# Performance work log

Hardware: AMD Instinct MI355X
Metric: run time of the kernel (lower is better)

The kernel has to match this reference:

```python
import jax, jax.numpy as jnp
import numpy as np

N_NODES = 50000
N_EDGES = 800000
N_GRAPHS = 128
IN, HID, OUT, CLS = 128, 128, 128, 10


def setup_inputs() -> dict:
    key = jax.random.key(0)
    ks = jax.random.split(key, 16)
    d = {}
    d["features"] = jax.random.normal(ks[0], (N_NODES, IN), jnp.float32)
    d["edge_src"] = jax.random.randint(ks[1], (N_EDGES,), 0, N_NODES)
    d["edge_dst"] = jax.random.randint(ks[2], (N_EDGES,), 0, N_NODES)
    d["graph_ids"] = jnp.sort(jax.random.randint(ks[3], (N_NODES,), 0, N_GRAPHS))

    def lin(k, i, o):
        return (jax.random.normal(k, (i, o), jnp.float32) / np.float32(np.sqrt(i)))

    dims = [(IN, HID), (HID, HID), (HID, OUT)]
    for l, (i, o) in enumerate(dims):
        d[f"Ws{l}"] = lin(ks[4 + 3 * l], i, o)
        d[f"Wn{l}"] = lin(ks[5 + 3 * l], i, o)
        d[f"b{l}"] = jnp.zeros((o,), jnp.float32)
    d["Wf"] = lin(ks[13], OUT, CLS)
    d["bf"] = jnp.zeros((CLS,), jnp.float32)
    return d


def _sage_mean_layer(h, edge_src, edge_dst, Ws, Wn, b, in_deg):
    # mean-aggregate in-neighbor features: gather at src, segment-sum at dst
    msg_sum = jax.ops.segment_sum(h[edge_src], edge_dst, num_segments=N_NODES)
    h_neigh = msg_sum / in_deg  # [N, d], zero-degree nodes divide by 1 -> 0
    return jax.nn.relu(h @ Ws + h_neigh @ Wn + b)


def reference(features, edge_src, edge_dst, graph_ids,
              Ws0, Wn0, b0, Ws1, Wn1, b1, Ws2, Wn2, b2, Wf, bf):
    ones = jnp.ones((N_EDGES,), jnp.float32)
    in_deg = jax.ops.segment_sum(ones, edge_dst, num_segments=N_NODES)
    in_deg = jnp.maximum(in_deg, 1.0)[:, None]  # [N, 1]

    h = features
    h = _sage_mean_layer(h, edge_src, edge_dst, Ws0, Wn0, b0, in_deg)
    h = _sage_mean_layer(h, edge_src, edge_dst, Ws1, Wn1, b1, in_deg)
    h = _sage_mean_layer(h, edge_src, edge_dst, Ws2, Wn2, b2, in_deg)

    # mean graph pooling over node segments
    node_ones = jnp.ones((N_NODES,), jnp.float32)
    counts = jax.ops.segment_sum(node_ones, graph_ids, num_segments=N_GRAPHS)
    counts = jnp.maximum(counts, 1.0)[:, None]
    pooled = jax.ops.segment_sum(h, graph_ids, num_segments=N_GRAPHS) / counts

    return pooled @ Wf + bf  # [N_GRAPHS, CLS]
```

## Files before the change

### kernel.cpp

```cpp
#include <hip/hip_runtime.h>

#define N_NODES  50000
#define N_EDGES  800000
#define N_GRAPHS 128
#define HD       128
#define K2       256
#define CLS      10
#define NB_SCAN  ((N_NODES + 255) / 256)
#define NPART    8
#define PSIZE    (N_NODES / NPART)
#define NBIN     400
#define CHUNK    (N_EDGES / NBIN)
#define PCAP     131072

typedef __attribute__((ext_vector_type(8))) _Float16 f16x8;
typedef __attribute__((ext_vector_type(4))) float f32x4;
typedef __attribute__((ext_vector_type(2))) float f32x2;

union U4H8 { uint4 u; _Float16 h[8]; };
union U2H4 { uint2 u; _Float16 h[4]; };

__device__ inline float h2f(unsigned short s) {
    union { unsigned short u; _Float16 h; } c; c.u = s; return (float)c.h;
}

__global__ __launch_bounds__(256) void k_init(const float* __restrict__ f,
                                              unsigned short* __restrict__ c0, unsigned char* __restrict__ f8,
                                              const float* __restrict__ Ws0, const float* __restrict__ Wn0,
                                              const float* __restrict__ Ws1, const float* __restrict__ Wn1,
                                              const float* __restrict__ Ws2, const float* __restrict__ Wn2,
                                              unsigned short* __restrict__ wt,
                                              int* __restrict__ zero_region, float* __restrict__ pooled,
                                              const int* __restrict__ gid, float* __restrict__ counts) {
    long long gi = (long long)blockIdx.x * 256 + threadIdx.x;
    if (gi < 800000) {
        int t = (int)gi;
        int row = t >> 4, c8 = (t & 15) * 8;
        const float* p = f + (size_t)row * HD + c8;
        float4 a = *(const float4*)p;
        float4 b = *(const float4*)(p + 4);
        U4H8 v;
        v.h[0] = (_Float16)a.x; v.h[1] = (_Float16)a.y;
        v.h[2] = (_Float16)a.z; v.h[3] = (_Float16)a.w;
        v.h[4] = (_Float16)b.x; v.h[5] = (_Float16)b.y;
        v.h[6] = (_Float16)b.z; v.h[7] = (_Float16)b.w;
        *(uint4*)(c0 + (size_t)row * K2 + c8) = v.u;
        int p0 = __builtin_amdgcn_cvt_pk_fp8_f32(a.x, a.y, 0, false);
        p0 = __builtin_amdgcn_cvt_pk_fp8_f32(a.z, a.w, p0, true);
        int p1 = __builtin_amdgcn_cvt_pk_fp8_f32(b.x, b.y, 0, false);
        p1 = __builtin_amdgcn_cvt_pk_fp8_f32(b.z, b.w, p1, true);
        *(uint2*)(f8 + (size_t)row * HD + c8) = make_uint2((unsigned)p0, (unsigned)p1);
        return;
    }
    gi -= 800000;
    if (gi < 3 * HD * K2) {
        int t = (int)gi;
        int l = t / (HD * K2), r = t % (HD * K2);
        int n = r / K2, k = r % K2;
        const float* Ws = (l == 0) ? Ws0 : (l == 1) ? Ws1 : Ws2;
        const float* Wn = (l == 0) ? Wn0 : (l == 1) ? Wn1 : Wn2;
        float w = (k < HD) ? Ws[k * HD + n] : Wn[(k - HD) * HD + n];
        union { unsigned short u; _Float16 h; } c;
        c.h = (_Float16)w;
        wt[t] = c.u;
        return;
    }
    gi -= 3 * HD * K2;
    if (gi < 50064) { zero_region[gi] = 0; return; }
    gi -= 50064;
    if (gi < N_GRAPHS * HD) { pooled[gi] = 0.f; return; }
    gi -= (long long)N_GRAPHS * HD;
    if (gi < N_GRAPHS) {
        int g = (int)gi;
        int lo = 0, hi = N_NODES;
        while (lo < hi) { int mid = (lo + hi) >> 1; if (gid[mid] < g) lo = mid + 1; else hi = mid; }
        int start = lo;
        lo = 0; hi = N_NODES;
        while (lo < hi) { int mid = (lo + hi) >> 1; if (gid[mid] <= g) lo = mid + 1; else hi = mid; }
        counts[g] = (float)(lo - start);
    }
}
#define INIT_THREADS (800000 + 3 * HD * K2 + 50064 + N_GRAPHS * HD + N_GRAPHS)

__global__ __launch_bounds__(256) void k_bin(const int* __restrict__ src, const int* __restrict__ dst,
                                             int2* __restrict__ stag, int* __restrict__ gcount) {
    __shared__ int lcount[NPART];
    __shared__ int lbase[NPART];
    const int tid = threadIdx.x;
    const int lane = tid & 63;
    const int lo = blockIdx.x * CHUNK;
    if (tid < NPART) lcount[tid] = 0;
    __syncthreads();
    for (int i = lo + tid; i < lo + CHUNK; i += 256) {
        int p = dst[i] / PSIZE;
#pragma unroll
        for (int q = 0; q < NPART; ++q) {
            unsigned long long m = __ballot(p == q);
            if (p == q) {
                int leader = __ffsll((long long)m) - 1;
                if (lane == leader) atomicAdd(&lcount[q], (int)__popcll(m));
            }
        }
    }
    __syncthreads();
    if (tid < NPART) {
        lbase[tid] = atomicAdd(&gcount[tid], lcount[tid]);
        lcount[tid] = 0;
    }
    __syncthreads();
    for (int i = lo + tid; i < lo + CHUNK; i += 256) {
        int d = dst[i];
        int p = d / PSIZE;
        int slot = 0;
#pragma unroll
        for (int q = 0; q < NPART; ++q) {
            unsigned long long m = __ballot(p == q);
            if (p == q) {
                int leader = __ffsll((long long)m) - 1;
                int rank = (int)__popcll(m & ((1ull << lane) - 1ull));
                int base;
                if (lane == leader) base = atomicAdd(&lcount[q], (int)__popcll(m));
                base = __shfl(base, leader);
                slot = base + rank;
            }
        }
        stag[(size_t)p * PCAP + lbase[p] + slot] = make_int2(src[i], d);
    }
}

__global__ __launch_bounds__(256) void k_deg2(const int2* __restrict__ stag, const int* __restrict__ gcount,
                                              int* __restrict__ deg) {
    const int part = blockIdx.x & (NPART - 1);
    const int blk = blockIdx.x >> 3;
    const int n = gcount[part];
    const int2* s = stag + (size_t)part * PCAP;
    for (int i = blk * 256 + threadIdx.x; i < n; i += 64 * 256)
        atomicAdd(&deg[s[i].y], 1);
}

__global__ __launch_bounds__(256) void k_fill2(const int2* __restrict__ stag, const int* __restrict__ gcount,
                                               int* __restrict__ cursor, int* __restrict__ eidx) {
    const int part = blockIdx.x & (NPART - 1);
    const int blk = blockIdx.x >> 3;
    const int n = gcount[part];
    const int2* s = stag + (size_t)part * PCAP;
    for (int i = blk * 256 + threadIdx.x; i < n; i += 64 * 256) {
        int2 e = s[i];
        int pos = atomicAdd(&cursor[e.y], 1);
        eidx[pos] = e.x;
    }
}

__global__ __launch_bounds__(256) void k_scan_part(const int* __restrict__ deg,
                                                   int* __restrict__ rowptr, int* __restrict__ bsum) {
    __shared__ int s[256];
    const int tid = threadIdx.x;
    const int i = blockIdx.x * 256 + tid;
    int v = (i < N_NODES) ? deg[i] : 0;
    s[tid] = v;
    __syncthreads();
    for (int off = 1; off < 256; off <<= 1) {
        int add = (tid >= off) ? s[tid - off] : 0;
        __syncthreads();
        s[tid] += add;
        __syncthreads();
    }
    if (i < N_NODES) rowptr[i] = s[tid] - v;
    if (tid == 255) bsum[blockIdx.x] = s[255];
}

__global__ __launch_bounds__(256) void k_scan_add(int* __restrict__ rowptr, const int* __restrict__ bsum,
                                                  int* __restrict__ cursor) {
    __shared__ int s[256];
    __shared__ int off_sh;
    const int tid = threadIdx.x;
    int v = (tid < NB_SCAN) ? bsum[tid] : 0;
    s[tid] = v;
    __syncthreads();
    for (int off = 1; off < 256; off <<= 1) {
        int add = (tid >= off) ? s[tid - off] : 0;
        __syncthreads();
        s[tid] += add;
        __syncthreads();
    }
    if (tid == blockIdx.x) off_sh = s[tid] - v;
    __syncthreads();
    const int i = blockIdx.x * 256 + tid;
    if (i < N_NODES) {
        int r = rowptr[i] + off_sh;
        rowptr[i] = r;
        cursor[i] = r;
    }
    if (blockIdx.x == 0 && tid == 0) rowptr[N_NODES] = N_EDGES;
}

__global__ __launch_bounds__(256) void k_gather(const unsigned char* __restrict__ h8,
                                                const int* __restrict__ rowptr,
                                                const int* __restrict__ eidx,
                                                unsigned short* __restrict__ msg) {
    const int node = (blockIdx.x * 256 + threadIdx.x) >> 6;
    const int lane = threadIdx.x & 63;
    if (node >= N_NODES) return;
    const int epar = lane >> 4;
    const int d0 = (lane & 15) * 8;
    const int beg = rowptr[node], end = rowptr[node + 1];
    float acc[8] = {0.f, 0.f, 0.f, 0.f, 0.f, 0.f, 0.f, 0.f};
    int j = beg + epar;
    for (; j + 12 < end; j += 16) {
        int s0 = eidx[j], s1 = eidx[j + 4], s2 = eidx[j + 8], s3 = eidx[j + 12];
        uint2 v0 = *(const uint2*)(h8 + (size_t)s0 * HD + d0);
        uint2 v1 = *(const uint2*)(h8 + (size_t)s1 * HD + d0);
        uint2 v2 = *(const uint2*)(h8 + (size_t)s2 * HD + d0);
        uint2 v3 = *(const uint2*)(h8 + (size_t)s3 * HD + d0);
        f32x2 e;
        e = __builtin_amdgcn_cvt_pk_f32_fp8(v0.x, false); acc[0] += e[0]; acc[1] += e[1];
        e = __builtin_amdgcn_cvt_pk_f32_fp8(v0.x, true);  acc[2] += e[0]; acc[3] += e[1];
        e = __builtin_amdgcn_cvt_pk_f32_fp8(v0.y, false); acc[4] += e[0]; acc[5] += e[1];
        e = __builtin_amdgcn_cvt_pk_f32_fp8(v0.y, true);  acc[6] += e[0]; acc[7] += e[1];
        e = __builtin_amdgcn_cvt_pk_f32_fp8(v1.x, false); acc[0] += e[0]; acc[1] += e[1];
        e = __builtin_amdgcn_cvt_pk_f32_fp8(v1.x, true);  acc[2] += e[0]; acc[3] += e[1];
        e = __builtin_amdgcn_cvt_pk_f32_fp8(v1.y, false); acc[4] += e[0]; acc[5] += e[1];
        e = __builtin_amdgcn_cvt_pk_f32_fp8(v1.y, true);  acc[6] += e[0]; acc[7] += e[1];
        e = __builtin_amdgcn_cvt_pk_f32_fp8(v2.x, false); acc[0] += e[0]; acc[1] += e[1];
        e = __builtin_amdgcn_cvt_pk_f32_fp8(v2.x, true);  acc[2] += e[0]; acc[3] += e[1];
        e = __builtin_amdgcn_cvt_pk_f32_fp8(v2.y, false); acc[4] += e[0]; acc[5] += e[1];
        e = __builtin_amdgcn_cvt_pk_f32_fp8(v2.y, true);  acc[6] += e[0]; acc[7] += e[1];
        e = __builtin_amdgcn_cvt_pk_f32_fp8(v3.x, false); acc[0] += e[0]; acc[1] += e[1];
        e = __builtin_amdgcn_cvt_pk_f32_fp8(v3.x, true);  acc[2] += e[0]; acc[3] += e[1];
        e = __builtin_amdgcn_cvt_pk_f32_fp8(v3.y, false); acc[4] += e[0]; acc[5] += e[1];
        e = __builtin_amdgcn_cvt_pk_f32_fp8(v3.y, true);  acc[6] += e[0]; acc[7] += e[1];
    }
    for (; j < end; j += 4) {
        uint2 v0 = *(const uint2*)(h8 + (size_t)eidx[j] * HD + d0);
        f32x2 e;
        e = __builtin_amdgcn_cvt_pk_f32_fp8(v0.x, false); acc[0] += e[0]; acc[1] += e[1];
        e = __builtin_amdgcn_cvt_pk_f32_fp8(v0.x, true);  acc[2] += e[0]; acc[3] += e[1];
        e = __builtin_amdgcn_cvt_pk_f32_fp8(v0.y, false); acc[4] += e[0]; acc[5] += e[1];
        e = __builtin_amdgcn_cvt_pk_f32_fp8(v0.y, true);  acc[6] += e[0]; acc[7] += e[1];
    }
#pragma unroll
    for (int i = 0; i < 8; ++i) {
        acc[i] += __shfl_xor(acc[i], 16);
        acc[i] += __shfl_xor(acc[i], 32);
    }
    if (epar == 0) {
        float inv = (end > beg) ? 1.0f / (float)(end - beg) : 0.f;
        U4H8 o;
#pragma unroll
        for (int i = 0; i < 8; ++i) o.h[i] = (_Float16)(acc[i] * inv);
        *(uint4*)(msg + (size_t)node * K2 + HD + d0) = o.u;
    }
}

__global__ __launch_bounds__(256) void k_sage(const unsigned short* __restrict__ hin,
                                              const unsigned short* __restrict__ wt,
                                              const float* __restrict__ bias,
                                              unsigned short* __restrict__ hout,
                                              unsigned char* __restrict__ hout8,
                                              int write16) {
    __shared__ _Float16 Ah[128 * 40];
    __shared__ _Float16 Bw[128 * 40];
    const int tid = threadIdx.x;
    const int wv = tid >> 6, lane = tid & 63;
    const int m0 = blockIdx.x * 128;
    const int m_off = (wv >> 1) * 64, n_off = (wv & 1) * 64;
    const int l15 = lane & 15, q = lane >> 4;

    f32x4 acc[4][4];
#pragma unroll
    for (int a = 0; a < 4; ++a)
#pragma unroll
        for (int b = 0; b < 4; ++b) acc[a][b] = (f32x4){0.f, 0.f, 0.f, 0.f};

#pragma unroll 1
    for (int kt = 0; kt < 8; ++kt) {
        const int k0 = kt * 32;
#pragma unroll
        for (int i = 0; i < 2; ++i) {
            int idx = tid + i * 256;
            int row = idx >> 2, kq = (idx & 3) * 8;
            int gm = m0 + row;
            uint4 va = make_uint4(0u, 0u, 0u, 0u);
            if (gm < N_NODES) va = *(const uint4*)(hin + (size_t)gm * K2 + k0 + kq);
            *(uint4*)&Ah[row * 40 + kq] = va;
            *(uint4*)&Bw[row * 40 + kq] = *(const uint4*)(wt + (size_t)row * K2 + k0 + kq);
        }
        __syncthreads();
        f16x8 hf[4], wf[4];
#pragma unroll
        for (int mt = 0; mt < 4; ++mt)
            hf[mt] = *(const f16x8*)&Ah[(m_off + mt * 16 + l15) * 40 + q * 8];
#pragma unroll
        for (int nt = 0; nt < 4; ++nt)
            wf[nt] = *(const f16x8*)&Bw[(n_off + nt * 16 + l15) * 40 + q * 8];
#pragma unroll
        for (int mt = 0; mt < 4; ++mt)
#pragma unroll
            for (int nt = 0; nt < 4; ++nt)
                acc[mt][nt] = __builtin_amdgcn_mfma_f32_16x16x32_f16(wf[nt], hf[mt], acc[mt][nt], 0, 0, 0);
        __syncthreads();
    }
#pragma unroll
    for (int nt = 0; nt < 4; ++nt) {
        int n = n_off + nt * 16 + q * 4;
        float4 bv = *(const float4*)(bias + n);
#pragma unroll
        for (int mt = 0; mt < 4; ++mt) {
            int m = m0 + m_off + mt * 16 + l15;
            if (m < N_NODES) {
                f32x4 a = acc[mt][nt];
                float r0 = fmaxf(a[0] + bv.x, 0.f);
                float r1 = fmaxf(a[1] + bv.y, 0.f);
                float r2 = fmaxf(a[2] + bv.z, 0.f);
                float r3 = fmaxf(a[3] + bv.w, 0.f);
                if (write16) {
                    U2H4 v;
                    v.h[0] = (_Float16)r0; v.h[1] = (_Float16)r1;
                    v.h[2] = (_Float16)r2; v.h[3] = (_Float16)r3;
                    *(uint2*)(hout + (size_t)m * K2 + n) = v.u;
                }
                int p = __builtin_amdgcn_cvt_pk_fp8_f32(r0, r1, 0, false);
                p = __builtin_amdgcn_cvt_pk_fp8_f32(r2, r3, p, true);
                *(unsigned int*)(hout8 + (size_t)m * HD + n) = (unsigned)p;
            }
        }
    }
}

__global__ __launch_bounds__(256) void k_pool(const unsigned char* __restrict__ h8,
                                              const int* __restrict__ gid,
                                              float* __restrict__ pooled) {
    const int p2 = (threadIdx.x & 63) * 2;
    const int sl = threadIdx.x >> 6;
    const int n0 = blockIdx.x * 128;
    float a0 = 0.f, a1 = 0.f;
    int cur = -1;
    for (int i = sl; i < 128; i += 4) {
        int n = n0 + i;
        if (n >= N_NODES) break;
        int g = gid[n];
        if (g != cur) {
            if (cur >= 0) {
                atomicAdd(&pooled[(size_t)cur * HD + p2], a0);
                atomicAdd(&pooled[(size_t)cur * HD + p2 + 1], a1);
            }
            a0 = 0.f; a1 = 0.f;
            cur = g;
        }
        unsigned short v = *(const unsigned short*)(h8 + (size_t)n * HD + p2);
        f32x2 e = __builtin_amdgcn_cvt_pk_f32_fp8((unsigned)v, false);
        a0 += e[0]; a1 += e[1];
    }
    if (cur >= 0) {
        atomicAdd(&pooled[(size_t)cur * HD + p2], a0);
        atomicAdd(&pooled[(size_t)cur * HD + p2 + 1], a1);
    }
}

__global__ __launch_bounds__(256) void k_final(const float* __restrict__ pooled,
                                               const float* __restrict__ counts,
                                               const float* __restrict__ Wf,
                                               const float* __restrict__ bf,
                                               float* __restrict__ out) {
    int t = blockIdx.x * 256 + threadIdx.x;
    if (t >= N_GRAPHS * CLS) return;
    int g = t / CLS, c = t % CLS;
    float inv = 1.0f / fmaxf(counts[g], 1.0f);
    float s = 0.f;
    for (int k = 0; k < HD; ++k) s += pooled[(size_t)g * HD + k] * Wf[k * CLS + c];
    out[t] = s * inv + bf[c];
}

extern "C" void kernel_launch(void* const* d_in, const int* in_sizes, int n_in,
                              void* d_out, int out_size, void* d_ws, size_t ws_size,
                              hipStream_t stream) {
    const float* features = (const float*)d_in[0];
    const int*   esrc     = (const int*)d_in[1];
    const int*   edst     = (const int*)d_in[2];
    const int*   gids     = (const int*)d_in[3];
    const float* bs[3]  = {(const float*)d_in[6], (const float*)d_in[9], (const float*)d_in[12]};
    const float* Wf = (const float*)d_in[13];
    const float* bfv = (const float*)d_in[14];
    float* out = (float*)d_out;

    int* deg_i  = (int*)d_ws;
    int* gcount = deg_i + 50000;
    int* rowptr = deg_i + 50064;
    int* cursor = rowptr + 50064;
    int* bsum   = cursor + 50048;
    int* eidx   = bsum + 256;
    int2* stag  = (int2*)(eidx + 800000);
    float* pooled = (float*)(stag + (size_t)NPART * PCAP);
    float* counts = pooled + N_GRAPHS * HD;
    unsigned short* C0 = (unsigned short*)(counts + 128);
    unsigned short* C1 = C0 + (size_t)N_NODES * K2;
    unsigned short* C2 = C1 + (size_t)N_NODES * K2;
    unsigned short* Wt = C2 + (size_t)N_NODES * K2;
    unsigned char* F0 = (unsigned char*)(Wt + 3 * HD * K2);
    unsigned char* F1 = F0 + (size_t)N_NODES * HD;
    unsigned char* F2 = F1 + (size_t)N_NODES * HD;

    k_init<<<(INIT_THREADS + 255) / 256, 256, 0, stream>>>(
        features, C0, F0,
        (const float*)d_in[4], (const float*)d_in[5],
        (const float*)d_in[7], (const float*)d_in[8],
        (const float*)d_in[10], (const float*)d_in[11],
        Wt, deg_i, pooled, gids, counts);

    k_bin<<<NBIN, 256, 0, stream>>>(esrc, edst, stag, gcount);
    k_deg2<<<NPART * 64, 256, 0, stream>>>(stag, gcount, deg_i);
    k_scan_part<<<NB_SCAN, 256, 0, stream>>>(deg_i, rowptr, bsum);
    k_scan_add<<<NB_SCAN, 256, 0, stream>>>(rowptr, bsum, cursor);
    k_fill2<<<NPART * 64, 256, 0, stream>>>(stag, gcount, cursor, eidx);

    unsigned short* C[4] = {C0, C1, C2, C0};
    unsigned char* F[4] = {F0, F1, F2, F0};
    for (int l = 0; l < 3; ++l) {
        k_gather<<<(N_NODES * 64 + 255) / 256, 256, 0, stream>>>(F[l], rowptr, eidx, C[l]);
        k_sage<<<(N_NODES + 127) / 128, 256, 0, stream>>>(
            C[l], Wt + (size_t)l * HD * K2, bs[l], C[l + 1], F[l + 1], (l < 2) ? 1 : 0);
    }

    k_pool<<<(N_NODES + 127) / 128, 256, 0, stream>>>(F0, gids, pooled);
    k_final<<<(N_GRAPHS * CLS + 255) / 256, 256, 0, stream>>>(pooled, counts, Wf, bfv, out);
}
```

Baseline: 358.2 us.

## Fuse init with binning, single-pass scan, double-buffered async-LDS GEMM staging

Merges the init and edge-binning kernels into one launch and counts degrees directly from dst during binning, removing the separate degree pass. The two-kernel scan becomes a single kernel whose blocks wait on flags set by earlier blocks. The SAGE GEMM now stages 64-wide K tiles with global_load_lds into double-buffered, XOR-swizzled LDS, so the next tile loads while MFMAs run on the current one. The scan's spin-wait assumes every scan block is resident at once, and the larger LDS buffers may lower occupancy.

```diff
diff --git a/kernel.cpp b/kernel.cpp
--- a/kernel.cpp
+++ b/kernel.cpp
@@ -20,19 +20,73 @@
 union U4H8 { uint4 u; _Float16 h[8]; };
 union U2H4 { uint2 u; _Float16 h[4]; };
 
-__device__ inline float h2f(unsigned short s) {
-    union { unsigned short u; _Float16 h; } c; c.u = s; return (float)c.h;
-}
-
-__global__ __launch_bounds__(256) void k_init(const float* __restrict__ f,
-                                              unsigned short* __restrict__ c0, unsigned char* __restrict__ f8,
-                                              const float* __restrict__ Ws0, const float* __restrict__ Wn0,
-                                              const float* __restrict__ Ws1, const float* __restrict__ Wn1,
-                                              const float* __restrict__ Ws2, const float* __restrict__ Wn2,
-                                              unsigned short* __restrict__ wt,
-                                              int* __restrict__ zero_region, float* __restrict__ pooled,
-                                              const int* __restrict__ gid, float* __restrict__ counts) {
-    long long gi = (long long)blockIdx.x * 256 + threadIdx.x;
+typedef const __attribute__((address_space(1))) void* gptr_t;
+typedef __attribute__((address_space(3))) void* lptr_t;
+#define GLOAD_LDS16(g, l) \
+    __builtin_amdgcn_global_load_lds((gptr_t)(g), (lptr_t)(l), 16, 0, 0)
+
+__global__ __launch_bounds__(256) void k_zero(int* __restrict__ z) {
+    int i = blockIdx.x * 256 + threadIdx.x;
+    if (i < 50008) z[i] = 0;
+}
+
+__global__ __launch_bounds__(256) void k_initbin(
+    const float* __restrict__ f, unsigned short* __restrict__ c0, unsigned char* __restrict__ f8,
+    const float* __restrict__ Ws0, const float* __restrict__ Wn0,
+    const float* __restrict__ Ws1, const float* __restrict__ Wn1,
+    const float* __restrict__ Ws2, const float* __restrict__ Wn2,
+    unsigned short* __restrict__ wt, float* __restrict__ pooled,
+    const int* __restrict__ gid, float* __restrict__ counts, int* __restrict__ bflag,
+    const int* __restrict__ src, const int* __restrict__ dst,
+    int2* __restrict__ stag, int* __restrict__ gcount, int* __restrict__ deg) {
+    if (blockIdx.x < NBIN) {
+        __shared__ int lcount[NPART];
+        __shared__ int lbase[NPART];
+        const int tid = threadIdx.x;
+        const int lane = tid & 63;
+        const int lo = blockIdx.x * CHUNK;
+        if (tid < NPART) lcount[tid] = 0;
+        __syncthreads();
+        for (int i = lo + tid; i < lo + CHUNK; i += 256) {
+            int d = dst[i];
+            atomicAdd(&deg[d], 1);
+            int p = d / PSIZE;
+#pragma unroll
+            for (int q = 0; q < NPART; ++q) {
+                unsigned long long m = __ballot(p == q);
+                if (p == q) {
+                    int leader = __ffsll((long long)m) - 1;
+                    if (lane == leader) atomicAdd(&lcount[q], (int)__popcll(m));
+                }
+            }
+        }
+        __syncthreads();
+        if (tid < NPART) {
+            lbase[tid] = atomicAdd(&gcount[tid], lcount[tid]);
+            lcount[tid] = 0;
+        }
+        __syncthreads();
+        for (int i = lo + tid; i < lo + CHUNK; i += 256) {
+            int d = dst[i];
+            int p = d / PSIZE;
+            int slot = 0;
+#pragma unroll
+            for (int q = 0; q < NPART; ++q) {
+                unsigned long long m = __ballot(p == q);
+                if (p == q) {
+                    int leader = __ffsll((long long)m) - 1;
+                    int rank = (int)__popcll(m & ((1ull << lane) - 1ull));
+                    int base;
+                    if (lane == leader) base = atomicAdd(&lcount[q], (int)__popcll(m));
+                    base = __shfl(base, leader);
+                    slot = base + rank;
+                }
+            }
+            stag[(size_t)p * PCAP + lbase[p] + slot] = make_int2(src[i], d);
+        }
+        return;
+    }
+    long long gi = (long long)(blockIdx.x - NBIN) * 256 + threadIdx.x;
     if (gi < 800000) {
         int t = (int)gi;
         int row = t >> 4, c8 = (t & 15) * 8;
@@ -66,8 +120,6 @@
         return;
     }
     gi -= 3 * HD * K2;
-    if (gi < 50064) { zero_region[gi] = 0; return; }
-    gi -= 50064;
     if (gi < N_GRAPHS * HD) { pooled[gi] = 0.f; return; }
     gi -= (long long)N_GRAPHS * HD;
     if (gi < N_GRAPHS) {
@@ -78,64 +130,52 @@
         lo = 0; hi = N_NODES;
         while (lo < hi) { int mid = (lo + hi) >> 1; if (gid[mid] <= g) lo = mid + 1; else hi = mid; }
         counts[g] = (float)(lo - start);
-    }
-}
-#define INIT_THREADS (800000 + 3 * HD * K2 + 50064 + N_GRAPHS * HD + N_GRAPHS)
-
-__global__ __launch_bounds__(256) void k_bin(const int* __restrict__ src, const int* __restrict__ dst,
-                                             int2* __restrict__ stag, int* __restrict__ gcount) {
-    __shared__ int lcount[NPART];
-    __shared__ int lbase[NPART];
+        return;
+    }
+    gi -= N_GRAPHS;
+    if (gi < 256) bflag[gi] = 0;
+}
+#define INIT_ITEMS (800000 + 3 * HD * K2 + N_GRAPHS * HD + N_GRAPHS + 256)
+#define INIT_BLOCKS ((INIT_ITEMS + 255) / 256)
+
+__global__ __launch_bounds__(256) void k_scan(const int* __restrict__ deg,
+                                              int* __restrict__ rowptr, int* __restrict__ cursor,
+                                              int* __restrict__ bsum, int* __restrict__ bflag) {
+    __shared__ int s[256];
+    __shared__ int r[256];
     const int tid = threadIdx.x;
-    const int lane = tid & 63;
-    const int lo = blockIdx.x * CHUNK;
-    if (tid < NPART) lcount[tid] = 0;
+    const int b = blockIdx.x;
+    const int i = b * 256 + tid;
+    int v = (i < N_NODES) ? deg[i] : 0;
+    s[tid] = v;
     __syncthreads();
-    for (int i = lo + tid; i < lo + CHUNK; i += 256) {
-        int p = dst[i] / PSIZE;
-#pragma unroll
-        for (int q = 0; q < NPART; ++q) {
-            unsigned long long m = __ballot(p == q);
-            if (p == q) {
-                int leader = __ffsll((long long)m) - 1;
-                if (lane == leader) atomicAdd(&lcount[q], (int)__popcll(m));
-            }
-        }
-    }
+    for (int off = 1; off < 256; off <<= 1) {
+        int add = (tid >= off) ? s[tid - off] : 0;
+        __syncthreads();
+        s[tid] += add;
+        __syncthreads();
+    }
+    if (tid == 255) {
+        __hip_atomic_store(&bsum[b], s[255], __ATOMIC_RELAXED, __HIP_MEMORY_SCOPE_AGENT);
+        __hip_atomic_store(&bflag[b], 1, __ATOMIC_RELEASE, __HIP_MEMORY_SCOPE_AGENT);
+    }
+    int agg = 0;
+    if (tid < b) {
+        while (__hip_atomic_load(&bflag[tid], __ATOMIC_ACQUIRE, __HIP_MEMORY_SCOPE_AGENT) == 0) {}
+        agg = __hip_atomic_load(&bsum[tid], __ATOMIC_RELAXED, __HIP_MEMORY_SCOPE_AGENT);
+    }
+    r[tid] = agg;
     __syncthreads();
-    if (tid < NPART) {
-        lbase[tid] = atomicAdd(&gcount[tid], lcount[tid]);
-        lcount[tid] = 0;
-    }
-    __syncthreads();
-    for (int i = lo + tid; i < lo + CHUNK; i += 256) {
-        int d = dst[i];
-        int p = d / PSIZE;
-        int slot = 0;
-#pragma unroll
-        for (int q = 0; q < NPART; ++q) {
-            unsigned long long m = __ballot(p == q);
-            if (p == q) {
-                int leader = __ffsll((long long)m) - 1;
-                int rank = (int)__popcll(m & ((1ull << lane) - 1ull));
-                int base;
-                if (lane == leader) base = atomicAdd(&lcount[q], (int)__popcll(m));
-                base = __shfl(base, leader);
-                slot = base + rank;
-            }
-        }
-        stag[(size_t)p * PCAP + lbase[p] + slot] = make_int2(src[i], d);
-    }
-}
-
-__global__ __launch_bounds__(256) void k_deg2(const int2* __restrict__ stag, const int* __restrict__ gcount,
-                                              int* __restrict__ deg) {
-    const int part = blockIdx.x & (NPART - 1);
-    const int blk = blockIdx.x >> 3;
-    const int n = gcount[part];
-    const int2* s = stag + (size_t)part * PCAP;
-    for (int i = blk * 256 + threadIdx.x; i < n; i += 64 * 256)
-        atomicAdd(&deg[s[i].y], 1);
+    for (int off = 128; off > 0; off >>= 1) {
+        if (tid < off) r[tid] += r[tid + off];
+        __syncthreads();
+    }
+    if (i < N_NODES) {
+        int val = r[0] + s[tid] - v;
+        rowptr[i] = val;
+        cursor[i] = val;
+    }
+    if (b == NB_SCAN - 1 && tid == 0) rowptr[N_NODES] = N_EDGES;
 }
 
 __global__ __launch_bounds__(256) void k_fill2(const int2* __restrict__ stag, const int* __restrict__ gcount,
@@ -149,49 +189,6 @@
         int pos = atomicAdd(&cursor[e.y], 1);
         eidx[pos] = e.x;
     }
-}
-
-__global__ __launch_bounds__(256) void k_scan_part(const int* __restrict__ deg,
-                                                   int* __restrict__ rowptr, int* __restrict__ bsum) {
-    __shared__ int s[256];
-    const int tid = threadIdx.x;
-    const int i = blockIdx.x * 256 + tid;
-    int v = (i < N_NODES) ? deg[i] : 0;
-    s[tid] = v;
-    __syncthreads();
-    for (int off = 1; off < 256; off <<= 1) {
-        int add = (tid >= off) ? s[tid - off] : 0;
-        __syncthreads();
-        s[tid] += add;
-        __syncthreads();
-    }
-    if (i < N_NODES) rowptr[i] = s[tid] - v;
-    if (tid == 255) bsum[blockIdx.x] = s[255];
-}
-
-__global__ __launch_bounds__(256) void k_scan_add(int* __restrict__ rowptr, const int* __restrict__ bsum,
-                                                  int* __restrict__ cursor) {
-    __shared__ int s[256];
-    __shared__ int off_sh;
-    const int tid = threadIdx.x;
-    int v = (tid < NB_SCAN) ? bsum[tid] : 0;
-    s[tid] = v;
-    __syncthreads();
-    for (int off = 1; off < 256; off <<= 1) {
-        int add = (tid >= off) ? s[tid - off] : 0;
-        __syncthreads();
-        s[tid] += add;
-        __syncthreads();
-    }
-    if (tid == blockIdx.x) off_sh = s[tid] - v;
-    __syncthreads();
-    const int i = blockIdx.x * 256 + tid;
-    if (i < N_NODES) {
-        int r = rowptr[i] + off_sh;
-        rowptr[i] = r;
-        cursor[i] = r;
-    }
-    if (blockIdx.x == 0 && tid == 0) rowptr[N_NODES] = N_EDGES;
 }
 
 __global__ __launch_bounds__(256) void k_gather(const unsigned char* __restrict__ h8,
@@ -258,8 +255,8 @@
                                               unsigned short* __restrict__ hout,
                                               unsigned char* __restrict__ hout8,
                                               int write16) {
-    __shared__ _Float16 Ah[128 * 40];
-    __shared__ _Float16 Bw[128 * 40];
+    __shared__ __align__(16) _Float16 Ah[2][128 * 64];
+    __shared__ __align__(16) _Float16 Bw[2][128 * 64];
     const int tid = threadIdx.x;
     const int wv = tid >> 6, lane = tid & 63;
     const int m0 = blockIdx.x * 128;
@@ -272,32 +269,50 @@
 #pragma unroll
         for (int b = 0; b < 4; ++b) acc[a][b] = (f32x4){0.f, 0.f, 0.f, 0.f};
 
-#pragma unroll 1
-    for (int kt = 0; kt < 8; ++kt) {
-        const int k0 = kt * 32;
-#pragma unroll
-        for (int i = 0; i < 2; ++i) {
+    auto stage = [&](int bsel, int kt) {
+        const int k0 = kt * 64;
+#pragma unroll
+        for (int i = 0; i < 4; ++i) {
             int idx = tid + i * 256;
-            int row = idx >> 2, kq = (idx & 3) * 8;
+            int row = idx >> 3, c = idx & 7;
+            int qs = (c ^ (row & 7)) * 8;
             int gm = m0 + row;
-            uint4 va = make_uint4(0u, 0u, 0u, 0u);
-            if (gm < N_NODES) va = *(const uint4*)(hin + (size_t)gm * K2 + k0 + kq);
-            *(uint4*)&Ah[row * 40 + kq] = va;
-            *(uint4*)&Bw[row * 40 + kq] = *(const uint4*)(wt + (size_t)row * K2 + k0 + kq);
-        }
-        __syncthreads();
-        f16x8 hf[4], wf[4];
+            if (gm < N_NODES)
+                GLOAD_LDS16(hin + (size_t)gm * K2 + k0 + qs, &Ah[bsel][idx * 8]);
+            GLOAD_LDS16(wt + (size_t)row * K2 + k0 + qs, &Bw[bsel][idx * 8]);
+        }
+    };
+
+    stage(0, 0);
+    __syncthreads();
+#pragma unroll
+    for (int kt = 0; kt < 4; ++kt) {
+        const int b = kt & 1;
+        if (kt < 3) stage(b ^ 1, kt + 1);
+        f16x8 hf[4][2], wf[4][2];
+#pragma unroll
+        for (int mt = 0; mt < 4; ++mt) {
+            const int row = m_off + mt * 16 + l15;
+            const int sw = row & 7;
+#pragma unroll
+            for (int ks = 0; ks < 2; ++ks)
+                hf[mt][ks] = *(const f16x8*)&Ah[b][row * 64 + (((ks * 4 + q) ^ sw) * 8)];
+        }
+#pragma unroll
+        for (int nt = 0; nt < 4; ++nt) {
+            const int row = n_off + nt * 16 + l15;
+            const int sw = row & 7;
+#pragma unroll
+            for (int ks = 0; ks < 2; ++ks)
+                wf[nt][ks] = *(const f16x8*)&Bw[b][row * 64 + (((ks * 4 + q) ^ sw) * 8)];
+        }
 #pragma unroll
         for (int mt = 0; mt < 4; ++mt)
-            hf[mt] = *(const f16x8*)&Ah[(m_off + mt * 16 + l15) * 40 + q * 8];
-#pragma unroll
-        for (int nt = 0; nt < 4; ++nt)
-            wf[nt] = *(const f16x8*)&Bw[(n_off + nt * 16 + l15) * 40 + q * 8];
-#pragma unroll
-        for (int mt = 0; mt < 4; ++mt)
-#pragma unroll
-            for (int nt = 0; nt < 4; ++nt)
-                acc[mt][nt] = __builtin_amdgcn_mfma_f32_16x16x32_f16(wf[nt], hf[mt], acc[mt][nt], 0, 0, 0);
+#pragma unroll
+            for (int nt = 0; nt < 4; ++nt) {
+                acc[mt][nt] = __builtin_amdgcn_mfma_f32_16x16x32_f16(wf[nt][0], hf[mt][0], acc[mt][nt], 0, 0, 0);
+                acc[mt][nt] = __builtin_amdgcn_mfma_f32_16x16x32_f16(wf[nt][1], hf[mt][1], acc[mt][nt], 0, 0, 0);
+            }
         __syncthreads();
     }
 #pragma unroll
@@ -388,7 +403,8 @@
     int* rowptr = deg_i + 50064;
     int* cursor = rowptr + 50064;
     int* bsum   = cursor + 50048;
-    int* eidx   = bsum + 256;
+    int* bflag  = bsum + 256;
+    int* eidx   = bflag + 256;
     int2* stag  = (int2*)(eidx + 800000);
     float* pooled = (float*)(stag + (size_t)NPART * PCAP);
     float* counts = pooled + N_GRAPHS * HD;
@@ -400,17 +416,17 @@
     unsigned char* F1 = F0 + (size_t)N_NODES * HD;
     unsigned char* F2 = F1 + (size_t)N_NODES * HD;
 
-    k_init<<<(INIT_THREADS + 255) / 256, 256, 0, stream>>>(
+    k_zero<<<196, 256, 0, stream>>>(deg_i);
+
+    k_initbin<<<NBIN + INIT_BLOCKS, 256, 0, stream>>>(
         features, C0, F0,
         (const float*)d_in[4], (const float*)d_in[5],
         (const float*)d_in[7], (const float*)d_in[8],
         (const float*)d_in[10], (const float*)d_in[11],
-        Wt, deg_i, pooled, gids, counts);
-
-    k_bin<<<NBIN, 256, 0, stream>>>(esrc, edst, stag, gcount);
-    k_deg2<<<NPART * 64, 256, 0, stream>>>(stag, gcount, deg_i);
-    k_scan_part<<<NB_SCAN, 256, 0, stream>>>(deg_i, rowptr, bsum);
-    k_scan_add<<<NB_SCAN, 256, 0, stream>>>(rowptr, bsum, cursor);
+        Wt, pooled, gids, counts, bflag,
+        esrc, edst, stag, gcount, deg_i);
+
+    k_scan<<<NB_SCAN, 256, 0, stream>>>(deg_i, rowptr, cursor, bsum, bflag);
     k_fill2<<<NPART * 64, 256, 0, stream>>>(stag, gcount, cursor, eidx);
 
     unsigned short* C[4] = {C0, C1, C2, C0};
```

Result: faster. 335.2 us (-6.4%).
